# Optimization experiments

Hardware: AMD Instinct MI355X
Metric: run time of the kernel (lower is better)

The kernel has to match this reference:

```python
import jax, jax.numpy as jnp
import numpy as np

N_NODES = 50000
N_EDGES = 600000
N_RELS = 19
D_IN = 128
D_HID = 64
D_OUT = 2


def setup_inputs() -> dict:
    key = jax.random.key(0)
    ks = jax.random.split(key, 10)
    feat = jax.random.normal(ks[0], (N_NODES, D_IN), dtype=jnp.float32)
    src = jax.random.randint(ks[1], (N_EDGES,), 0, N_NODES)
    dst = jax.random.randint(ks[2], (N_EDGES,), 0, N_NODES)
    etype = jax.random.randint(ks[3], (N_EDGES,), 0, N_RELS)
    s1 = 1.0 / np.sqrt(D_IN)
    s2 = 1.0 / np.sqrt(D_HID)
    W1 = jax.random.normal(ks[4], (N_RELS, D_IN, D_HID), dtype=jnp.float32) * s1
    loop1 = jax.random.normal(ks[5], (D_IN, D_HID), dtype=jnp.float32) * s1
    b1 = jnp.zeros((D_HID,), dtype=jnp.float32)
    W2 = jax.random.normal(ks[6], (N_RELS, D_HID, D_OUT), dtype=jnp.float32) * s2
    loop2 = jax.random.normal(ks[7], (D_HID, D_OUT), dtype=jnp.float32) * s2
    b2 = jnp.zeros((D_OUT,), dtype=jnp.float32)
    return {"feat": feat, "W1": W1, "loop1": loop1, "b1": b1,
            "W2": W2, "loop2": loop2, "b2": b2,
            "src": src, "dst": dst, "etype": etype}


def _rel_graph_conv(h, W, loop_w, bias, src, dst, etype, activation):
    # Per-relation transform of all nodes: [N, R, O]; then gather per edge.
    # (num_rels * out_feat is small, so this is cheaper than gathering W per edge.)
    transformed = jnp.einsum('nd,rdo->nro', h, W)
    msg = transformed[src, etype]                      # [E, O] edge messages
    agg = jax.ops.segment_sum(msg, dst, num_segments=h.shape[0])  # scatter-add
    out = agg + h @ loop_w + bias                      # self-loop + bias
    if activation is not None:
        out = activation(out)
    return out


def reference(feat, W1, loop1, b1, W2, loop2, b2, src, dst, etype):
    h = _rel_graph_conv(feat, W1, loop1, b1, src, dst, etype, jax.nn.relu)
    h = _rel_graph_conv(h, W2, loop2, b2, src, dst, etype, None)
    return h
```

## Files before the change

kernel.cpp:

```cpp
#include <hip/hip_runtime.h>

#define N_NODES 50000
#define N_EDGES 600000
#define N_RELS  19
#define D_IN    128
#define D_HID   64
#define D_OUT   2
#define EDGE_TILES ((N_EDGES + 127) / 128 + N_RELS)
#define SL_BLOCKS  ((N_NODES + 63) / 64)
#define PREP_ELEMS (N_RELS * D_HID * D_IN + 48 * 64 + D_HID * D_IN)
#define PREP_BLOCKS ((PREP_ELEMS + 255) / 256)

typedef unsigned short u16;
typedef unsigned int   u32;
typedef __attribute__((ext_vector_type(8))) short sfrag;
typedef __attribute__((ext_vector_type(4))) float f32x4;

__device__ __forceinline__ u16 f2bf(float f){
  union { float f; u32 i; } v; v.f = f;
  u32 r = v.i + 0x7fffu + ((v.i >> 16) & 1u);
  return (u16)(r >> 16);
}
__device__ __forceinline__ float bf2f(u16 u){
  union { u32 i; float f; } v; v.i = ((u32)u) << 16; return v.f;
}

__global__ __launch_bounds__(256) void k_fused_pre(const float* __restrict__ feat,
                                                   u16* __restrict__ featb,
                                                   const int* __restrict__ et,
                                                   const int* __restrict__ dst,
                                                   int* __restrict__ hist_rel,
                                                   int* __restrict__ hist_dst){
  int i = blockIdx.x * 256 + threadIdx.x;
  float2 f = ((const float2*)feat)[i];
  ((u32*)featb)[i] = (u32)f2bf(f.x) | ((u32)f2bf(f.y) << 16);
  if (blockIdx.x < (N_EDGES + 255) / 256) {
    __shared__ int lh[N_RELS];
    int tid = threadIdx.x;
    if (tid < N_RELS) lh[tid] = 0;
    __syncthreads();
    int e = blockIdx.x * 256 + tid;
    if (e < N_EDGES) {
      atomicAdd(&lh[et[e]], 1);
      atomicAdd(&hist_dst[dst[e]], 1);
    }
    __syncthreads();
    if (tid < N_RELS && lh[tid]) atomicAdd(&hist_rel[tid], lh[tid]);
  }
}

__global__ __launch_bounds__(256) void k_alloc_scan(
    const int* __restrict__ hist_dst, int* __restrict__ dstart,
    int* __restrict__ cur_dst, int* __restrict__ gcnt,
    const int* __restrict__ hist_rel, int* __restrict__ offs,
    int* __restrict__ toff, int* __restrict__ cur_rel,
    const float* __restrict__ W1, const float* __restrict__ loop1,
    const float* __restrict__ W2, u16* __restrict__ W1Tb,
    u16* __restrict__ loop1Tb, u16* __restrict__ W2allT){
  if (blockIdx.x >= 197) {
    int idx = (blockIdx.x - 197) * 256 + threadIdx.x;
    const int T1 = N_RELS * D_HID * D_IN;
    const int T2c = T1 + 48 * 64;
    const int T3 = T2c + D_HID * D_IN;
    if (idx < T1) {
      int r = idx / (D_HID * D_IN);
      int t = idx - r * (D_HID * D_IN);
      int j = t >> 7, d = t & 127;
      W1Tb[idx] = f2bf(W1[(r * D_IN + d) * D_HID + j]);
    } else if (idx < T2c) {
      int k2 = idx - T1;
      int n = k2 >> 6, k = k2 & 63;
      float val = 0.f;
      if (n < N_RELS * D_OUT) {
        int r = n >> 1, o = n & 1;
        val = W2[(r * D_HID + k) * D_OUT + o];
      }
      W2allT[k2] = f2bf(val);
    } else if (idx < T3) {
      int k2 = idx - T2c;
      int j = k2 >> 7, d = k2 & 127;
      loop1Tb[k2] = f2bf(loop1[d * D_HID + j]);
    }
    return;
  }
  if (blockIdx.x == 196) {
    if (threadIdx.x == 0) {
      int acc = 0, tacc = 0;
      offs[0] = 0; toff[0] = 0;
      for (int r = 0; r < N_RELS; ++r) {
        cur_rel[r] = acc;
        int c = hist_rel[r];
        acc += c;                offs[r + 1] = acc;
        tacc += (c + 127) >> 7;  toff[r + 1] = tacc;
      }
    }
    return;
  }
  __shared__ int wbase[4];
  int tid = threadIdx.x, lane = tid & 63, wv = tid >> 6;
  int n = blockIdx.x * 256 + tid;
  int v = (n < N_NODES) ? hist_dst[n] : 0;
  int x = v;
  #pragma unroll
  for (int o = 1; o < 64; o <<= 1) { int u = __shfl_up(x, o); if (lane >= o) x += u; }
  if (lane == 63) wbase[wv] = atomicAdd(gcnt, x);
  __syncthreads();
  int start = wbase[wv] + x - v;
  if (n < N_NODES) { dstart[n] = start; cur_dst[n] = start; }
}

__global__ __launch_bounds__(256) void k_scatter_rel(const int* __restrict__ et,
                                                     int* __restrict__ cursor,
                                                     int* __restrict__ perm){
  __shared__ int lh[N_RELS], base[N_RELS];
  int tid = threadIdx.x;
  if (tid < N_RELS) lh[tid] = 0;
  __syncthreads();
  int e = blockIdx.x * 256 + tid;
  int r = 0, my = 0;
  bool valid = e < N_EDGES;
  if (valid) { r = et[e]; my = atomicAdd(&lh[r], 1); }
  __syncthreads();
  if (tid < N_RELS && lh[tid]) base[tid] = atomicAdd(&cursor[tid], lh[tid]);
  __syncthreads();
  if (valid) perm[base[r] + my] = e;
}

__global__ __launch_bounds__(256) void k_se1(
    const u16* __restrict__ featb, const u16* __restrict__ W1Tb,
    const u16* __restrict__ loop1Tb, const float* __restrict__ b1,
    const int* __restrict__ src, const int* __restrict__ dst,
    const int* __restrict__ perm, const int* __restrict__ offs,
    const int* __restrict__ toff, int* __restrict__ cur_dst,
    u16* __restrict__ msgbuf, float* __restrict__ agg1f){
  __shared__ __align__(16) u16 Bls[64][136];
  __shared__ __align__(16) u16 msg[128][72];
  __shared__ int posIds[128];
  int tid = threadIdx.x, lane = tid & 63, w = tid >> 6;
  int r16 = lane & 15, c4 = lane >> 4;

  if (blockIdx.x >= EDGE_TILES) {
    int base = (blockIdx.x - EDGE_TILES) * 64;
    { int j = tid >> 2, seg = tid & 3;
      const uint4* g = (const uint4*)(loop1Tb + j * 128) + seg * 4;
      uint4* d = (uint4*)&Bls[j][seg * 32];
      d[0] = g[0]; d[1] = g[1]; d[2] = g[2]; d[3] = g[3]; }
    int arow = base + w * 16 + r16; if (arow >= N_NODES) arow = N_NODES - 1;
    sfrag aF[4];
    #pragma unroll
    for (int kk = 0; kk < 4; ++kk)
      aF[kk] = *(const sfrag*)(featb + (size_t)arow * D_IN + kk * 32 + c4 * 8);
    __syncthreads();
    #pragma unroll
    for (int ct = 0; ct < 4; ++ct) {
      f32x4 acc = {0.f, 0.f, 0.f, 0.f};
      #pragma unroll
      for (int kk = 0; kk < 4; ++kk) {
        sfrag bF = *(const sfrag*)&Bls[ct * 16 + r16][kk * 32 + c4 * 8];
        acc = __builtin_amdgcn_mfma_f32_16x16x32_bf16(aF[kk], bF, acc, 0, 0, 0);
      }
      int col = ct * 16 + r16;
      float bias = b1[col];
      #pragma unroll
      for (int reg = 0; reg < 4; ++reg) {
        int orow = base + w * 16 + c4 * 4 + reg;
        if (orow < N_NODES) agg1f[(size_t)orow * D_HID + col] = acc[reg] + bias;
      }
    }
    return;
  }

  int b = blockIdx.x;
  unsigned long long mm = __ballot((lane < N_RELS) && (b >= toff[lane + 1]));
  int rel = __popcll(mm);
  if (rel >= N_RELS) return;
  int ts = offs[rel] + ((b - toff[rel]) << 7);
  int vc = offs[rel + 1] - ts; if (vc > 128) vc = 128;

  int myPos = -1;
  if (tid < 128 && tid < vc) {
    int e = perm[ts + tid];
    myPos = atomicAdd(&cur_dst[dst[e]], 1);
  }
  {
    int j = tid >> 2, seg = tid & 3;
    const uint4* g = (const uint4*)(W1Tb + ((size_t)rel * 64 + j) * 128) + seg * 4;
    uint4* d = (uint4*)&Bls[j][seg * 32];
    d[0] = g[0]; d[1] = g[1]; d[2] = g[2]; d[3] = g[3];
  }
  sfrag aF[2][4];
  #pragma unroll
  for (int mt = 0; mt < 2; ++mt) {
    int row = w * 32 + mt * 16 + r16;
    int rr = row < vc ? row : vc - 1;
    int s = src[perm[ts + rr]];
    const u16* ap = featb + (size_t)s * D_IN + c4 * 8;
    #pragma unroll
    for (int kk = 0; kk < 4; ++kk)
      aF[mt][kk] = *(const sfrag*)(ap + kk * 32);
  }
  __syncthreads();
  #pragma unroll
  for (int ct = 0; ct < 4; ++ct) {
    sfrag bF[4];
    #pragma unroll
    for (int kk = 0; kk < 4; ++kk)
      bF[kk] = *(const sfrag*)&Bls[ct * 16 + r16][kk * 32 + c4 * 8];
    #pragma unroll
    for (int mt = 0; mt < 2; ++mt) {
      f32x4 acc = {0.f, 0.f, 0.f, 0.f};
      #pragma unroll
      for (int kk = 0; kk < 4; ++kk)
        acc = __builtin_amdgcn_mfma_f32_16x16x32_bf16(aF[mt][kk], bF[kk], acc, 0, 0, 0);
      #pragma unroll
      for (int reg = 0; reg < 4; ++reg) {
        float v = acc[reg];
        float o = __shfl_xor(v, 1);
        float lo = (lane & 1) ? o : v;
        float hi = (lane & 1) ? v : o;
        u32 pk = (u32)f2bf(lo) | ((u32)f2bf(hi) << 16);
        if (!(lane & 1)) {
          int orow = w * 32 + mt * 16 + c4 * 4 + reg;
          *(u32*)&msg[orow][ct * 16 + r16] = pk;
        }
      }
    }
  }
  if (tid < 128) posIds[tid] = myPos;
  __syncthreads();
  { int row = tid >> 1, half = tid & 1;
    int pos = posIds[row];
    if (pos >= 0) {
      const uint4* mr = (const uint4*)&msg[row][half * 32];
      uint4* d = (uint4*)(msgbuf + (size_t)pos * D_HID + half * 32);
      d[0] = mr[0]; d[1] = mr[1]; d[2] = mr[2]; d[3] = mr[3];
    } }
}

__global__ __launch_bounds__(256) void k_agg_relu_self2(
    const u16* __restrict__ msgbuf, const int* __restrict__ dstart,
    const int* __restrict__ cnt, const float* __restrict__ agg1f,
    const float* __restrict__ loop2, const float* __restrict__ b2,
    u16* __restrict__ h1b, float* __restrict__ out){
  int wv = threadIdx.x >> 6, lane = threadIdx.x & 63;
  int n = blockIdx.x * 4 + wv;
  int s = dstart[n], epos = s + cnt[n];
  int h = lane >> 5, c = lane & 31;
  float a0 = 0.f, a1 = 0.f;
  for (int i = s + h; i < epos; i += 2) {
    u32 v = ((const u32*)msgbuf)[(size_t)i * 32 + c];
    a0 += bf2f((u16)(v & 0xffffu));
    a1 += bf2f((u16)(v >> 16));
  }
  a0 += __shfl_down(a0, 32);
  a1 += __shfl_down(a1, 32);
  float p0 = 0.f, p1 = 0.f;
  if (h == 0) {
    float2 sl = ((const float2*)(agg1f + (size_t)n * D_HID))[c];
    float v0 = a0 + sl.x, v1 = a1 + sl.y;
    v0 = v0 > 0.f ? v0 : 0.f;
    v1 = v1 > 0.f ? v1 : 0.f;
    ((u32*)h1b)[(size_t)n * 32 + c] = (u32)f2bf(v0) | ((u32)f2bf(v1) << 16);
    float2 w0 = ((const float2*)loop2)[2 * c];
    float2 w1 = ((const float2*)loop2)[2 * c + 1];
    p0 = v0 * w0.x + v1 * w1.x;
    p1 = v0 * w0.y + v1 * w1.y;
  }
  #pragma unroll
  for (int off = 16; off; off >>= 1) {
    p0 += __shfl_down(p0, off);
    p1 += __shfl_down(p1, off);
  }
  if (lane == 0) {
    out[n * 2]     = p0 + b2[0];
    out[n * 2 + 1] = p1 + b2[1];
  }
}

__global__ __launch_bounds__(256) void k_t2(
    const u16* __restrict__ h1b, const u16* __restrict__ W2allT,
    float* __restrict__ T2){
  __shared__ __align__(16) u16 Bls[48][72];
  int tid = threadIdx.x, lane = tid & 63, w = tid >> 6;
  int r16 = lane & 15, c4 = lane >> 4;
  for (int idx = tid; idx < 48 * 8; idx += 256) {
    int row = idx >> 3, q = idx & 7;
    ((uint4*)&Bls[row][0])[q] = ((const uint4*)W2allT)[idx];
  }
  int base = blockIdx.x * 64;
  int arow = base + w * 16 + r16; if (arow >= N_NODES) arow = N_NODES - 1;
  sfrag aF[2];
  #pragma unroll
  for (int kk = 0; kk < 2; ++kk)
    aF[kk] = *(const sfrag*)(h1b + (size_t)arow * D_HID + kk * 32 + c4 * 8);
  __syncthreads();
  #pragma unroll
  for (int ct = 0; ct < 3; ++ct) {
    f32x4 acc = {0.f, 0.f, 0.f, 0.f};
    #pragma unroll
    for (int kk = 0; kk < 2; ++kk) {
      sfrag bF = *(const sfrag*)&Bls[ct * 16 + r16][kk * 32 + c4 * 8];
      acc = __builtin_amdgcn_mfma_f32_16x16x32_bf16(aF[kk], bF, acc, 0, 0, 0);
    }
    int col = ct * 16 + r16;
    if (col < N_RELS * D_OUT) {
      #pragma unroll
      for (int reg = 0; reg < 4; ++reg) {
        int orow = base + w * 16 + c4 * 4 + reg;
        if (orow < N_NODES) T2[(size_t)orow * 40 + col] = acc[reg];
      }
    }
  }
}

__global__ __launch_bounds__(256) void k_edge2(
    const float* __restrict__ T2, const int* __restrict__ src,
    const int* __restrict__ dst, const int* __restrict__ et,
    float* __restrict__ out){
  int e = blockIdx.x * 256 + threadIdx.x;
  if (e >= N_EDGES) return;
  int s = src[e], d = dst[e], r = et[e];
  float2 v = *(const float2*)(T2 + (size_t)s * 40 + r * 2);
  atomicAdd(&out[d * 2],     v.x);
  atomicAdd(&out[d * 2 + 1], v.y);
}

extern "C" void kernel_launch(void* const* d_in, const int* in_sizes, int n_in,
                              void* d_out, int out_size, void* d_ws, size_t ws_size,
                              hipStream_t stream){
  const float* feat  = (const float*)d_in[0];
  const float* W1    = (const float*)d_in[1];
  const float* loop1 = (const float*)d_in[2];
  const float* b1    = (const float*)d_in[3];
  const float* W2    = (const float*)d_in[4];
  const float* loop2 = (const float*)d_in[5];
  const float* b2    = (const float*)d_in[6];
  const int* src     = (const int*)d_in[7];
  const int* dst     = (const int*)d_in[8];
  const int* et      = (const int*)d_in[9];
  float* out = (float*)d_out;

  char* w = (char*)d_ws;
  u16*   W1Tb     = (u16*)(w);
  u16*   W2allT   = (u16*)(w + 311296);
  u16*   loop1Tb  = (u16*)(w + 350208);
  int*   hist_rel = (int*)(w + 366592);
  int*   gcnt     = (int*)(w + 366720);
  int*   hist_dst = (int*)(w + 366848);
  int*   offs     = (int*)(w + 566848);
  int*   toff     = (int*)(w + 566976);
  int*   cur_rel  = (int*)(w + 567104);
  int*   dstart   = (int*)(w + 567232);
  int*   cur_dst  = (int*)(w + 767232);
  int*   perm     = (int*)(w + 967232);
  u16*   featb    = (u16*)(w + 3367232);
  float* T2f      = (float*)(w + 3367232);
  float* agg1f    = (float*)(w + 16167232);
  u16*   h1b      = (u16*)(w + 28967232);
  u16*   msgbuf   = (u16*)(w + 35367232);

  hipMemsetAsync(w + 366592, 0, 200256, stream);
  k_fused_pre     <<<12500, 256, 0, stream>>>(feat, featb, et, dst, hist_rel, hist_dst);
  k_alloc_scan    <<<197 + PREP_BLOCKS, 256, 0, stream>>>(
                      hist_dst, dstart, cur_dst, gcnt, hist_rel, offs, toff, cur_rel,
                      W1, loop1, W2, W1Tb, loop1Tb, W2allT);
  k_scatter_rel   <<<2344,  256, 0, stream>>>(et, cur_rel, perm);
  k_se1           <<<EDGE_TILES + SL_BLOCKS, 256, 0, stream>>>(
                      featb, W1Tb, loop1Tb, b1, src, dst, perm, offs, toff,
                      cur_dst, msgbuf, agg1f);
  k_agg_relu_self2<<<12500, 256, 0, stream>>>(msgbuf, dstart, hist_dst, agg1f,
                                              loop2, b2, h1b, out);
  k_t2            <<<SL_BLOCKS, 256, 0, stream>>>(h1b, W2allT, T2f);
  k_edge2         <<<(N_EDGES + 255) / 256, 256, 0, stream>>>(T2f, src, dst, et, out);
}
```

Baseline: 337.8 us.

## Bucket edges by source block and relation; replace layer-2 atomics with CSR gather

Edges are now sorted into segments keyed by (src>>9, relation) rather than by relation alone, and per-tile segment/start tables are built in the scan kernel. This makes each edge tile's source feature gathers more local, and tiles are remapped across XCDs for L2 locality. Layer 1 also records a packed (src, rel) per dst-sorted slot, which lets layer 2 gather per destination node instead of scattering float atomics per edge. The layer-1 self-loop result is stored in bf16 via an LDS staging pass. The cost is more segments, which means more partially filled tiles, and a serial scan over segments.

```diff
diff --git a/kernel.cpp b/kernel.cpp
--- a/kernel.cpp
+++ b/kernel.cpp
@@ -6,7 +6,10 @@
 #define D_IN    128
 #define D_HID   64
 #define D_OUT   2
-#define EDGE_TILES ((N_EDGES + 127) / 128 + N_RELS)
+#define BSH     9
+#define NB      ((N_NODES + 511) >> 9)
+#define NSEG    (NB * N_RELS)
+#define NTILE_CAP (NSEG + (N_EDGES + 127) / 128)
 #define SL_BLOCKS  ((N_NODES + 63) / 64)
 #define PREP_ELEMS (N_RELS * D_HID * D_IN + 48 * 64 + D_HID * D_IN)
 #define PREP_BLOCKS ((PREP_ELEMS + 255) / 256)
@@ -24,36 +27,33 @@
 __device__ __forceinline__ float bf2f(u16 u){
   union { u32 i; float f; } v; v.i = ((u32)u) << 16; return v.f;
 }
+__device__ __forceinline__ u32 pack2(float lo, float hi){
+  return (u32)f2bf(lo) | ((u32)f2bf(hi) << 16);
+}
 
 __global__ __launch_bounds__(256) void k_fused_pre(const float* __restrict__ feat,
                                                    u16* __restrict__ featb,
+                                                   const int* __restrict__ src,
                                                    const int* __restrict__ et,
                                                    const int* __restrict__ dst,
-                                                   int* __restrict__ hist_rel,
+                                                   int* __restrict__ seg_hist,
                                                    int* __restrict__ hist_dst){
   int i = blockIdx.x * 256 + threadIdx.x;
   float2 f = ((const float2*)feat)[i];
   ((u32*)featb)[i] = (u32)f2bf(f.x) | ((u32)f2bf(f.y) << 16);
-  if (blockIdx.x < (N_EDGES + 255) / 256) {
-    __shared__ int lh[N_RELS];
-    int tid = threadIdx.x;
-    if (tid < N_RELS) lh[tid] = 0;
-    __syncthreads();
-    int e = blockIdx.x * 256 + tid;
-    if (e < N_EDGES) {
-      atomicAdd(&lh[et[e]], 1);
-      atomicAdd(&hist_dst[dst[e]], 1);
-    }
-    __syncthreads();
-    if (tid < N_RELS && lh[tid]) atomicAdd(&hist_rel[tid], lh[tid]);
+  if (i < N_EDGES) {
+    int key = (src[i] >> BSH) * N_RELS + et[i];
+    atomicAdd(&seg_hist[key * 16], 1);
+    atomicAdd(&hist_dst[dst[i]], 1);
   }
 }
 
 __global__ __launch_bounds__(256) void k_alloc_scan(
     const int* __restrict__ hist_dst, int* __restrict__ dstart,
     int* __restrict__ cur_dst, int* __restrict__ gcnt,
-    const int* __restrict__ hist_rel, int* __restrict__ offs,
-    int* __restrict__ toff, int* __restrict__ cur_rel,
+    const int* __restrict__ seg_hist, int* __restrict__ seg_off,
+    int* __restrict__ cur_seg, int* __restrict__ ntile,
+    int* __restrict__ tseg, int* __restrict__ tstart,
     const float* __restrict__ W1, const float* __restrict__ loop1,
     const float* __restrict__ W2, u16* __restrict__ W1Tb,
     u16* __restrict__ loop1Tb, u16* __restrict__ W2allT){
@@ -84,16 +84,29 @@
     return;
   }
   if (blockIdx.x == 196) {
-    if (threadIdx.x == 0) {
-      int acc = 0, tacc = 0;
-      offs[0] = 0; toff[0] = 0;
-      for (int r = 0; r < N_RELS; ++r) {
-        cur_rel[r] = acc;
-        int c = hist_rel[r];
-        acc += c;                offs[r + 1] = acc;
-        tacc += (c + 127) >> 7;  toff[r + 1] = tacc;
-      }
-    }
+    __shared__ int se_s[256], st_s[256];
+    int tid = threadIdx.x;
+    const int PER = (NSEG + 255) / 256;
+    int lo = tid * PER, hi = lo + PER; if (hi > NSEG) hi = NSEG; if (lo > NSEG) lo = NSEG;
+    int se = 0, st = 0;
+    for (int i = lo; i < hi; ++i) { int c = seg_hist[i * 16]; se += c; st += (c + 127) >> 7; }
+    se_s[tid] = se; st_s[tid] = st;
+    __syncthreads();
+    if (tid == 0) {
+      int a = 0, b = 0;
+      for (int j = 0; j < 256; ++j) { int x = se_s[j], y = st_s[j]; se_s[j] = a; st_s[j] = b; a += x; b += y; }
+      ntile[0] = b;
+    }
+    __syncthreads();
+    int eo = se_s[tid], to = st_s[tid];
+    for (int i = lo; i < hi; ++i) {
+      int c = seg_hist[i * 16];
+      seg_off[i] = eo; cur_seg[i * 16] = eo;
+      int nt = (c + 127) >> 7;
+      for (int k = 0; k < nt; ++k) { tseg[to + k] = i; tstart[to + k] = eo + (k << 7); }
+      eo += c; to += nt;
+    }
+    if (hi == NSEG) seg_off[NSEG] = eo;
     return;
   }
   __shared__ int wbase[4];
@@ -109,38 +122,33 @@
   if (n < N_NODES) { dstart[n] = start; cur_dst[n] = start; }
 }
 
-__global__ __launch_bounds__(256) void k_scatter_rel(const int* __restrict__ et,
-                                                     int* __restrict__ cursor,
-                                                     int* __restrict__ perm){
-  __shared__ int lh[N_RELS], base[N_RELS];
-  int tid = threadIdx.x;
-  if (tid < N_RELS) lh[tid] = 0;
-  __syncthreads();
-  int e = blockIdx.x * 256 + tid;
-  int r = 0, my = 0;
-  bool valid = e < N_EDGES;
-  if (valid) { r = et[e]; my = atomicAdd(&lh[r], 1); }
-  __syncthreads();
-  if (tid < N_RELS && lh[tid]) base[tid] = atomicAdd(&cursor[tid], lh[tid]);
-  __syncthreads();
-  if (valid) perm[base[r] + my] = e;
+__global__ __launch_bounds__(256) void k_scatter(const int* __restrict__ src,
+                                                 const int* __restrict__ et,
+                                                 int* __restrict__ cur_seg,
+                                                 int* __restrict__ perm){
+  int e = blockIdx.x * 256 + threadIdx.x;
+  if (e >= N_EDGES) return;
+  int key = (src[e] >> BSH) * N_RELS + et[e];
+  int p = atomicAdd(&cur_seg[key * 16], 1);
+  perm[p] = e;
 }
 
 __global__ __launch_bounds__(256) void k_se1(
     const u16* __restrict__ featb, const u16* __restrict__ W1Tb,
     const u16* __restrict__ loop1Tb, const float* __restrict__ b1,
     const int* __restrict__ src, const int* __restrict__ dst,
-    const int* __restrict__ perm, const int* __restrict__ offs,
-    const int* __restrict__ toff, int* __restrict__ cur_dst,
-    u16* __restrict__ msgbuf, float* __restrict__ agg1f){
+    const int* __restrict__ perm, const int* __restrict__ seg_off,
+    const int* __restrict__ ntile_p, const int* __restrict__ tseg,
+    const int* __restrict__ tstart, int* __restrict__ cur_dst,
+    int* __restrict__ srel, u16* __restrict__ msgbuf, u16* __restrict__ agg1b){
   __shared__ __align__(16) u16 Bls[64][136];
   __shared__ __align__(16) u16 msg[128][72];
   __shared__ int posIds[128];
   int tid = threadIdx.x, lane = tid & 63, w = tid >> 6;
   int r16 = lane & 15, c4 = lane >> 4;
 
-  if (blockIdx.x >= EDGE_TILES) {
-    int base = (blockIdx.x - EDGE_TILES) * 64;
+  if (blockIdx.x >= NTILE_CAP) {
+    int base = (blockIdx.x - NTILE_CAP) * 64;
     { int j = tid >> 2, seg = tid & 3;
       const uint4* g = (const uint4*)(loop1Tb + j * 128) + seg * 4;
       uint4* d = (uint4*)&Bls[j][seg * 32];
@@ -163,29 +171,49 @@
       float bias = b1[col];
       #pragma unroll
       for (int reg = 0; reg < 4; ++reg) {
-        int orow = base + w * 16 + c4 * 4 + reg;
-        if (orow < N_NODES) agg1f[(size_t)orow * D_HID + col] = acc[reg] + bias;
+        float v = acc[reg] + bias;
+        float o = __shfl_xor(v, 1);
+        if (!(lane & 1)) {
+          int orow = w * 16 + c4 * 4 + reg;
+          *(u32*)&msg[orow][col] = pack2(v, o);
+        }
       }
     }
+    __syncthreads();
+    { int row = tid >> 2, q = tid & 3;
+      int n = base + row;
+      if (n < N_NODES) {
+        uint4 a0 = ((const uint4*)&msg[row][0])[q * 2];
+        uint4 a1 = ((const uint4*)&msg[row][0])[q * 2 + 1];
+        uint4* d = (uint4*)(agg1b + (size_t)n * D_HID + q * 16);
+        d[0] = a0; d[1] = a1;
+      } }
     return;
   }
 
-  int b = blockIdx.x;
-  unsigned long long mm = __ballot((lane < N_RELS) && (b >= toff[lane + 1]));
-  int rel = __popcll(mm);
-  if (rel >= N_RELS) return;
-  int ts = offs[rel] + ((b - toff[rel]) << 7);
-  int vc = offs[rel + 1] - ts; if (vc > 128) vc = 128;
+  int nt = *ntile_p;
+  int pb = blockIdx.x;
+  if (pb >= nt) return;
+  int q8 = nt >> 3, r8 = nt & 7;
+  int xcd = pb & 7, idx = pb >> 3;
+  int b = (xcd < r8 ? xcd * (q8 + 1) : r8 * (q8 + 1) + (xcd - r8) * q8) + idx;
+
+  int seg = tseg[b];
+  int ts  = tstart[b];
+  int vc  = seg_off[seg + 1] - ts; if (vc > 128) vc = 128;
+  int rel = seg % N_RELS;
 
   int myPos = -1;
   if (tid < 128 && tid < vc) {
     int e = perm[ts + tid];
+    int s2 = src[e];
     myPos = atomicAdd(&cur_dst[dst[e]], 1);
+    srel[myPos] = (s2 << 5) | rel;
   }
   {
-    int j = tid >> 2, seg = tid & 3;
-    const uint4* g = (const uint4*)(W1Tb + ((size_t)rel * 64 + j) * 128) + seg * 4;
-    uint4* d = (uint4*)&Bls[j][seg * 32];
+    int j = tid >> 2, seg2 = tid & 3;
+    const uint4* g = (const uint4*)(W1Tb + ((size_t)rel * 64 + j) * 128) + seg2 * 4;
+    uint4* d = (uint4*)&Bls[j][seg2 * 32];
     d[0] = g[0]; d[1] = g[1]; d[2] = g[2]; d[3] = g[3];
   }
   sfrag aF[2][4];
@@ -216,12 +244,9 @@
       for (int reg = 0; reg < 4; ++reg) {
         float v = acc[reg];
         float o = __shfl_xor(v, 1);
-        float lo = (lane & 1) ? o : v;
-        float hi = (lane & 1) ? v : o;
-        u32 pk = (u32)f2bf(lo) | ((u32)f2bf(hi) << 16);
         if (!(lane & 1)) {
           int orow = w * 32 + mt * 16 + c4 * 4 + reg;
-          *(u32*)&msg[orow][ct * 16 + r16] = pk;
+          *(u32*)&msg[orow][ct * 16 + r16] = pack2(v, o);
         }
       }
     }
@@ -239,7 +264,7 @@
 
 __global__ __launch_bounds__(256) void k_agg_relu_self2(
     const u16* __restrict__ msgbuf, const int* __restrict__ dstart,
-    const int* __restrict__ cnt, const float* __restrict__ agg1f,
+    const int* __restrict__ cnt, const u16* __restrict__ agg1b,
     const float* __restrict__ loop2, const float* __restrict__ b2,
     u16* __restrict__ h1b, float* __restrict__ out){
   int wv = threadIdx.x >> 6, lane = threadIdx.x & 63;
@@ -256,8 +281,9 @@
   a1 += __shfl_down(a1, 32);
   float p0 = 0.f, p1 = 0.f;
   if (h == 0) {
-    float2 sl = ((const float2*)(agg1f + (size_t)n * D_HID))[c];
-    float v0 = a0 + sl.x, v1 = a1 + sl.y;
+    u32 sv = ((const u32*)agg1b)[(size_t)n * 32 + c];
+    float v0 = a0 + bf2f((u16)(sv & 0xffffu));
+    float v1 = a1 + bf2f((u16)(sv >> 16));
     v0 = v0 > 0.f ? v0 : 0.f;
     v1 = v1 > 0.f ? v1 : 0.f;
     ((u32*)h1b)[(size_t)n * 32 + c] = (u32)f2bf(v0) | ((u32)f2bf(v1) << 16);
@@ -313,16 +339,28 @@
   }
 }
 
-__global__ __launch_bounds__(256) void k_edge2(
-    const float* __restrict__ T2, const int* __restrict__ src,
-    const int* __restrict__ dst, const int* __restrict__ et,
+__global__ __launch_bounds__(256) void k_fin(
+    const float* __restrict__ T2, const int* __restrict__ srel,
+    const int* __restrict__ dstart, const int* __restrict__ cnt,
     float* __restrict__ out){
-  int e = blockIdx.x * 256 + threadIdx.x;
-  if (e >= N_EDGES) return;
-  int s = src[e], d = dst[e], r = et[e];
-  float2 v = *(const float2*)(T2 + (size_t)s * 40 + r * 2);
-  atomicAdd(&out[d * 2],     v.x);
-  atomicAdd(&out[d * 2 + 1], v.y);
+  int wv = threadIdx.x >> 6, lane = threadIdx.x & 63;
+  int n = blockIdx.x * 4 + wv;
+  int s = dstart[n], c = cnt[n];
+  float ax = 0.f, ay = 0.f;
+  for (int i = lane; i < c; i += 64) {
+    int sr = srel[s + i];
+    const float* p = T2 + (size_t)(sr >> 5) * 40 + (sr & 31) * 2;
+    ax += p[0]; ay += p[1];
+  }
+  #pragma unroll
+  for (int off = 32; off; off >>= 1) {
+    ax += __shfl_down(ax, off);
+    ay += __shfl_down(ay, off);
+  }
+  if (lane == 0) {
+    out[n * 2]     += ax;
+    out[n * 2 + 1] += ay;
+  }
 }
 
 extern "C" void kernel_launch(void* const* d_in, const int* in_sizes, int n_in,
@@ -343,33 +381,36 @@
   char* w = (char*)d_ws;
   u16*   W1Tb     = (u16*)(w);
   u16*   W2allT   = (u16*)(w + 311296);
-  u16*   loop1Tb  = (u16*)(w + 350208);
-  int*   hist_rel = (int*)(w + 366592);
-  int*   gcnt     = (int*)(w + 366720);
-  int*   hist_dst = (int*)(w + 366848);
-  int*   offs     = (int*)(w + 566848);
-  int*   toff     = (int*)(w + 566976);
-  int*   cur_rel  = (int*)(w + 567104);
-  int*   dstart   = (int*)(w + 567232);
-  int*   cur_dst  = (int*)(w + 767232);
-  int*   perm     = (int*)(w + 967232);
-  u16*   featb    = (u16*)(w + 3367232);
-  float* T2f      = (float*)(w + 3367232);
-  float* agg1f    = (float*)(w + 16167232);
-  u16*   h1b      = (u16*)(w + 28967232);
-  u16*   msgbuf   = (u16*)(w + 35367232);
-
-  hipMemsetAsync(w + 366592, 0, 200256, stream);
-  k_fused_pre     <<<12500, 256, 0, stream>>>(feat, featb, et, dst, hist_rel, hist_dst);
+  u16*   loop1Tb  = (u16*)(w + 317440);
+  int*   seg_hist = (int*)(w + 333824);
+  int*   gcnt     = (int*)(w + 452992);
+  int*   hist_dst = (int*)(w + 453056);
+  int*   seg_off  = (int*)(w + 653056);
+  int*   cur_seg  = (int*)(w + 660544);
+  int*   ntile    = (int*)(w + 779712);
+  int*   tseg     = (int*)(w + 779776);
+  int*   tstart   = (int*)(w + 806016);
+  int*   dstart   = (int*)(w + 832256);
+  int*   cur_dst  = (int*)(w + 1032256);
+  int*   perm     = (int*)(w + 1232256);
+  int*   srel     = (int*)(w + 3632256);
+  u16*   featb    = (u16*)(w + 6032256);
+  float* T2f      = (float*)(w + 6032256);
+  u16*   agg1b    = (u16*)(w + 18832256);
+  u16*   h1b      = (u16*)(w + 25232256);
+  u16*   msgbuf   = (u16*)(w + 31632256);
+
+  hipMemsetAsync(w + 333824, 0, 319232, stream);
+  k_fused_pre     <<<12500, 256, 0, stream>>>(feat, featb, src, et, dst, seg_hist, hist_dst);
   k_alloc_scan    <<<197 + PREP_BLOCKS, 256, 0, stream>>>(
-                      hist_dst, dstart, cur_dst, gcnt, hist_rel, offs, toff, cur_rel,
-                      W1, loop1, W2, W1Tb, loop1Tb, W2allT);
-  k_scatter_rel   <<<2344,  256, 0, stream>>>(et, cur_rel, perm);
-  k_se1           <<<EDGE_TILES + SL_BLOCKS, 256, 0, stream>>>(
-                      featb, W1Tb, loop1Tb, b1, src, dst, perm, offs, toff,
-                      cur_dst, msgbuf, agg1f);
-  k_agg_relu_self2<<<12500, 256, 0, stream>>>(msgbuf, dstart, hist_dst, agg1f,
+                      hist_dst, dstart, cur_dst, gcnt, seg_hist, seg_off, cur_seg,
+                      ntile, tseg, tstart, W1, loop1, W2, W1Tb, loop1Tb, W2allT);
+  k_scatter       <<<2344,  256, 0, stream>>>(src, et, cur_seg, perm);
+  k_se1           <<<NTILE_CAP + SL_BLOCKS, 256, 0, stream>>>(
+                      featb, W1Tb, loop1Tb, b1, src, dst, perm, seg_off, ntile,
+                      tseg, tstart, cur_dst, srel, msgbuf, agg1b);
+  k_agg_relu_self2<<<12500, 256, 0, stream>>>(msgbuf, dstart, hist_dst, agg1b,
                                               loop2, b2, h1b, out);
   k_t2            <<<SL_BLOCKS, 256, 0, stream>>>(h1b, W2allT, T2f);
-  k_edge2         <<<(N_EDGES + 255) / 256, 256, 0, stream>>>(T2f, src, dst, et, out);
-}
+  k_fin           <<<12500, 256, 0, stream>>>(T2f, srel, dstart, hist_dst, out);
+}
```

Result: faster. 304.7 us (-9.8%).
